# Performance work log

Measured on AMD Instinct MI355X. Metric: run time of the kernel, lower is better.

## Reference

```python
import jax, jax.numpy as jnp
import numpy as np
from jax import lax

HID = 512
NEG = -1e30

def conv2d(x, w, pad):
    # x: [N,C,H,W], w: [O,I,kh,kw]
    return lax.conv_general_dilated(x, w, (1, 1), [(pad, pad), (pad, pad)],
                                    dimension_numbers=('NCHW', 'OIHW', 'NCHW'))

def maxpool3s2p1(x):
    return lax.reduce_window(x, -jnp.inf, lax.max, (1, 1, 3, 3), (1, 1, 2, 2),
                             [(0, 0), (0, 0), (1, 1), (1, 1)])

def setup_inputs() -> dict:
    key = jax.random.key(0)
    ks = jax.random.split(key, 12)
    N, B = 128, 16
    gid = jnp.repeat(jnp.arange(B), N // B).astype(jnp.float32)  # sorted group ids
    rois = jnp.concatenate([gid[:, None], jax.random.uniform(ks[0], (N, 4))], axis=1)
    interact_feat = jax.random.normal(ks[1], (N, 2304, 1, 16, 16), jnp.float32)
    bbox_feat = jax.random.normal(ks[2], (N, 1024, 4, 7, 7), jnp.float32)
    s = lambda k, sh: jax.random.normal(k, sh, jnp.float32) * 0.02
    return {
        'rois': rois,
        'interact_feat': interact_feat,
        'bbox_feat': bbox_feat,
        'w_reduce': s(ks[3], (HID, 2304, 1, 1)),
        'w_rsize': s(ks[4], (HID, HID, 3, 3)),
        'wq': s(ks[5], (HID, HID, 3, 3)),
        'wk': s(ks[6], (HID, HID, 3, 3)),
        'wv': s(ks[7], (HID, HID, 3, 3)),
        'w1': s(ks[8], (HID, HID, 3, 3)),
        'gamma': jnp.ones((HID,), jnp.float32),
        'beta': jnp.zeros((HID,), jnp.float32),
        'w_fc': s(ks[9], (HID, 2 * HID)),
    }

def reference(rois, interact_feat, bbox_feat, w_reduce, w_rsize, wq, wk, wv, w1, gamma, beta, w_fc):
    f = interact_feat[:, :, 0]                      # squeeze(2): [N,2304,16,16]
    f = jax.nn.relu(conv2d(f, w_reduce, 0))         # [N,512,16,16]
    f = conv2d(f, w_rsize, 0)                       # no padding -> [N,512,14,14]
    f = maxpool3s2p1(f)                             # [N,512,7,7]

    gid = rois[:, 0].astype(jnp.int32)
    mask = gid[:, None] == gid[None, :]             # [N,N] same-group mask (vectorizes ragged loop)

    q = conv2d(f, wq, 1)
    k = conv2d(f, wk, 1)
    v = conv2d(f, wv, 1)
    # per-pixel attention across rois within each group
    att = jnp.einsum('ichw,jchw->ijhw', q, k) / jnp.sqrt(jnp.asarray(HID, f.dtype))
    att = jnp.where(mask[:, :, None, None], att, NEG)
    att = jax.nn.softmax(att, axis=1)               # softmax over key rois (dim=1)
    virt = jnp.einsum('ijhw,jchw->ichw', att, v)    # [N,512,7,7]

    # GroupNorm(1, C): normalize over (C,H,W), per-channel affine
    mu = virt.mean(axis=(1, 2, 3), keepdims=True)
    var = virt.var(axis=(1, 2, 3), keepdims=True)
    virt = (virt - mu) / jnp.sqrt(var + 1e-5)
    virt = virt * gamma[None, :, None, None] + beta[None, :, None, None]
    virt = jax.nn.relu(virt)
    virt = conv2d(virt, w1, 1)                      # dropout = identity in eval

    ho = (f + virt).mean(axis=(2, 3))               # gap1 -> [N,512]
    ob = bbox_feat.mean(axis=(2, 3, 4))             # gap2 -> [N,1024]
    ob = jax.nn.relu(ob @ w_fc.T)                   # fc1 -> [N,512]
    return jnp.concatenate([ho, ob], axis=1)        # [N,1024]
```

## Files before the change

kernel.cpp:

```cpp
#include <hip/hip_runtime.h>
#include <hip/hip_bf16.h>
#include <math.h>

typedef __bf16 bf16;
typedef __bf16 v8bf __attribute__((ext_vector_type(8)));
typedef float f32x4 __attribute__((ext_vector_type(4)));

#define GLDS16(g, l) __builtin_amdgcn_global_load_lds( \
    (const __attribute__((address_space(1))) void*)(g), \
    (__attribute__((address_space(3))) void*)(l), 16, 0, 0)

__device__ __forceinline__ int xcd_swz(int bid, int nwg) {
  int xcd = bid & 7, off = bid >> 3;
  int q = nwg >> 3, r = nwg & 7;
  return (xcd < r ? xcd * (q + 1) : r * (q + 1) + (xcd - r) * q) + off;
}

#define SBZ __builtin_amdgcn_sched_barrier(0)
#define BARR __builtin_amdgcn_s_barrier()

#define RD_B8(SLOTB) do { \
  _Pragma("unroll") for (int _j = 0; _j < 4; ++_j) \
  _Pragma("unroll") for (int _kk = 0; _kk < 2; ++_kk) { \
    int _r = (wn & 1) * 64 + _j * 16 + l15; \
    int _c = (_kk * 64 + kq) ^ ((_r & 7) << 4); \
    bfr[_j][_kk] = *(const v8bf*)((SLOTB) + _r * 128 + _c); } } while (0)

#define RD_A4(SLOTA, CL) do { \
  _Pragma("unroll") for (int _f = 0; _f < 2; ++_f) \
  _Pragma("unroll") for (int _kk = 0; _kk < 2; ++_kk) { \
    int _r = (CL) * 32 + _f * 16 + l15; \
    int _c = (_kk * 64 + kq) ^ ((_r & 7) << 4); \
    af[_f][_kk] = *(const v8bf*)((SLOTA) + _r * 128 + _c); } } while (0)

#define MMA16(CL) do { \
  __builtin_amdgcn_s_setprio(1); \
  _Pragma("unroll") for (int _f = 0; _f < 2; ++_f) \
  _Pragma("unroll") for (int _j = 0; _j < 4; ++_j) \
  _Pragma("unroll") for (int _kk = 0; _kk < 2; ++_kk) \
    acc[(CL)*2 + _f][_j] = __builtin_amdgcn_mfma_f32_16x16x32_bf16( \
        af[_f][_kk], bfr[_j][_kk], acc[(CL)*2 + _f][_j], 0, 0, 0); \
  __builtin_amdgcn_s_setprio(0); } while (0)

#define VM4 asm volatile("s_waitcnt vmcnt(4)" ::: "memory")
#define VM0 asm volatile("s_waitcnt vmcnt(0)" ::: "memory")

#define PH8_ITER(STGA, STGB, NIT)                                        \
  {                                                                      \
    int t1k = 2 * iv + 1, t2k = 2 * iv + 2, t3k = 2 * iv + 3;            \
    bool s2 = (iv + 1 < (NIT));                                          \
    RD_B8(bslot0); RD_A4(aslot0, 0); STGA(0, t1k, 1);                    \
    SBZ; BARR; SBZ; MMA16(0); SBZ; BARR;                                 \
    RD_A4(aslot0, 1); STGA(1, t1k, 1);                                   \
    SBZ; BARR; SBZ; MMA16(1); SBZ; BARR;                                 \
    RD_A4(aslot0, 2); if (s2) STGB(0, t2k, 0);                           \
    SBZ; BARR; SBZ; MMA16(2); SBZ; BARR;                                 \
    RD_A4(aslot0, 3); if (s2) STGB(1, t2k, 0);                           \
    SBZ; BARR; SBZ; MMA16(3); SBZ;                                       \
    if (s2) { VM4; } else { VM0; }                                       \
    BARR;                                                                \
    RD_B8(bslot1); RD_A4(aslot1, 0); if (s2) STGA(0, t2k, 0);            \
    SBZ; BARR; SBZ; MMA16(0); SBZ; BARR;                                 \
    RD_A4(aslot1, 1); if (s2) STGA(1, t2k, 0);                           \
    SBZ; BARR; SBZ; MMA16(1); SBZ; BARR;                                 \
    RD_A4(aslot1, 2); if (s2) STGB(0, t3k, 1);                           \
    SBZ; BARR; SBZ; MMA16(2); SBZ; BARR;                                 \
    RD_A4(aslot1, 3); if (s2) STGB(1, t3k, 1);                           \
    SBZ; BARR; SBZ; MMA16(3); SBZ;                                       \
    if (s2) { VM4; } else { VM0; }                                       \
    BARR;                                                                \
  }

__global__ __launch_bounds__(512, 2)
void k_gemm_reduce(const bf16* __restrict__ A, const bf16* __restrict__ B,
                   bf16* __restrict__ f1, int mbase)
{
  extern __shared__ char lds[];
  const int s = xcd_swz(blockIdx.x, gridDim.x);
  const int by = s & 1, bx = s >> 1;
  const int t = threadIdx.x, lane = t & 63, w = t >> 6;
  const int wm = w >> 2, wn = w & 3;
  const int l15 = lane & 15, kq = (lane >> 4) << 4;
  const int tr64 = t >> 3;
  const int lb = ((t & 7) << 4) ^ ((tr64 & 7) << 4);
  const int t16 = t * 16;
  const char* aslot0 = lds + wm * 16384;
  const char* aslot1 = lds + 65536 + wm * 16384;
  const char* bslot0 = lds + 32768 + (wn >> 1) * 16384;
  const char* bslot1 = lds + 98304 + (wn >> 1) * 16384;
  const char* paA[2][2]; const char* paB[2][2];
  #pragma unroll
  for (int h = 0; h < 2; ++h)
    #pragma unroll
    for (int c = 0; c < 2; ++c) {
      paA[h][c] = (const char*)A + (size_t)(bx * 256 + h * 128 + c * 64 + tr64) * 4608 + lb;
      paB[h][c] = (const char*)B + (size_t)(by * 256 + h * 128 + c * 64 + tr64) * 4608 + lb;
    }
  #define GR_STGA(h, kt, d) do { \
    GLDS16(paA[h][0] + (size_t)(kt) * 128, lds + (d) * 65536 + (h) * 16384 + t16); \
    GLDS16(paA[h][1] + (size_t)(kt) * 128, lds + (d) * 65536 + (h) * 16384 + 8192 + t16); } while (0)
  #define GR_STGB(h, kt, d) do { \
    GLDS16(paB[h][0] + (size_t)(kt) * 128, lds + (d) * 65536 + 32768 + (h) * 16384 + t16); \
    GLDS16(paB[h][1] + (size_t)(kt) * 128, lds + (d) * 65536 + 32768 + (h) * 16384 + 8192 + t16); } while (0)

  f32x4 acc[8][4] = {};
  v8bf bfr[4][2], af[2][2];
  GR_STGB(0, 0, 0); GR_STGB(1, 0, 0); GR_STGA(0, 0, 0); GR_STGA(1, 0, 0);
  GR_STGB(0, 1, 1); GR_STGB(1, 1, 1);
  VM4; BARR;
  for (int iv = 0; iv < 18; ++iv) PH8_ITER(GR_STGA, GR_STGB, 18);
  const int rbase = (lane >> 4) << 2, cl = lane & 15;
  #pragma unroll
  for (int i = 0; i < 8; ++i)
    #pragma unroll
    for (int j = 0; j < 4; ++j)
      #pragma unroll
      for (int r = 0; r < 4; ++r) {
        int row = mbase + bx * 256 + wm * 128 + i * 16 + rbase + r;
        int col = by * 256 + wn * 64 + j * 16 + cl;
        f1[(size_t)row * 512 + col] = (bf16)fmaxf(acc[i][j][r], 0.f);
      }
}

__global__ __launch_bounds__(512, 2)
void k_conv_rsize(const bf16* __restrict__ f1, const bf16* __restrict__ wt,
                  bf16* __restrict__ f14)
{
  extern __shared__ char lds[];
  const int s = xcd_swz(blockIdx.x, gridDim.x);
  const int by = s & 1, bx = s >> 1;
  const int t = threadIdx.x, lane = t & 63, w = t >> 6;
  const int wm = w >> 2, wn = w & 3;
  const int l15 = lane & 15, kq = (lane >> 4) << 4;
  const int tr64 = t >> 3;
  const int lb = ((t & 7) << 4) ^ ((tr64 & 7) << 4);
  const int t16 = t * 16;
  const char* aslot0 = lds + wm * 16384;
  const char* aslot1 = lds + 65536 + wm * 16384;
  const char* bslot0 = lds + 32768 + (wn >> 1) * 16384;
  const char* bslot1 = lds + 98304 + (wn >> 1) * 16384;
  int ab[2][2]; const char* pwB[2][2];
  #pragma unroll
  for (int h = 0; h < 2; ++h)
    #pragma unroll
    for (int c = 0; c < 2; ++c) {
      int m = bx * 256 + h * 128 + c * 64 + tr64;
      int n = m / 196, rem = m - n * 196;
      int y = rem / 14, x = rem - 14 * (rem / 14);
      ab[h][c] = n * 256 + y * 16 + x;
      pwB[h][c] = (const char*)wt + (size_t)(by * 256 + h * 128 + c * 64 + tr64) * 1024 + lb;
    }
  const char* f1c = (const char*)f1 + lb;
  #define CR_STGA(h, kt, d) do { \
    int _tap = (kt) >> 3, _ko = ((kt) & 7) << 7; \
    int _dy = (_tap * 11) >> 5, _dx = _tap - _dy * 3; \
    int _df = (_dy * 16 + _dx) << 10; \
    GLDS16(f1c + ((size_t)ab[h][0] << 10) + _df + _ko, lds + (d) * 65536 + (h) * 16384 + t16); \
    GLDS16(f1c + ((size_t)ab[h][1] << 10) + _df + _ko, lds + (d) * 65536 + (h) * 16384 + 8192 + t16); } while (0)
  #define CR_STGB(h, kt, d) do { \
    int _tap = (kt) >> 3, _ko = ((kt) & 7) << 7; \
    GLDS16(pwB[h][0] + (size_t)_tap * 524288 + _ko, lds + (d) * 65536 + 32768 + (h) * 16384 + t16); \
    GLDS16(pwB[h][1] + (size_t)_tap * 524288 + _ko, lds + (d) * 65536 + 32768 + (h) * 16384 + 8192 + t16); } while (0)

  f32x4 acc[8][4] = {};
  v8bf bfr[4][2], af[2][2];
  CR_STGB(0, 0, 0); CR_STGB(1, 0, 0); CR_STGA(0, 0, 0); CR_STGA(1, 0, 0);
  CR_STGB(0, 1, 1); CR_STGB(1, 1, 1);
  VM4; BARR;
  for (int iv = 0; iv < 36; ++iv) PH8_ITER(CR_STGA, CR_STGB, 36);
  const int rbase = (lane >> 4) << 2, cl = lane & 15;
  #pragma unroll
  for (int i = 0; i < 8; ++i)
    #pragma unroll
    for (int j = 0; j < 4; ++j)
      #pragma unroll
      for (int r = 0; r < 4; ++r) {
        int row = bx * 256 + wm * 128 + i * 16 + rbase + r;
        int col = by * 256 + wn * 64 + j * 16 + cl;
        f14[(size_t)row * 512 + col] = (bf16)acc[i][j][r];
      }
}

#define RING_COMPUTE() do { \
  v8bf b_[4], a_[4]; \
  _Pragma("unroll") for (int _j = 0; _j < 4; ++_j) { \
    int _lr = _j * 16 + l15; \
    int _c = (wn * 64 + colb) ^ ((_lr & 7) << 4); \
    b_[_j] = *(const v8bf*)(s0 + 16384 + _lr * 128 + _c); } \
  _Pragma("unroll") for (int _i = 0; _i < 4; ++_i) { \
    int _lr = _i * 16 + l15; \
    int _c = (wm * 64 + colb) ^ ((_lr & 7) << 4); \
    a_[_i] = *(const v8bf*)(s0 + _lr * 128 + _c); } \
  __builtin_amdgcn_s_setprio(1); \
  _Pragma("unroll") for (int _i = 0; _i < 4; ++_i) \
  _Pragma("unroll") for (int _j = 0; _j < 4; ++_j) \
    acc[_i][_j] = __builtin_amdgcn_mfma_f32_16x16x32_bf16(a_[_i], b_[_j], acc[_i][_j], 0, 0, 0); \
  __builtin_amdgcn_s_setprio(0); \
  _Pragma("unroll") for (int _i = 0; _i < 4; ++_i) { \
    int _lr = (_i + 4) * 16 + l15; \
    int _c = (wm * 64 + colb) ^ ((_lr & 7) << 4); \
    a_[_i] = *(const v8bf*)(s0 + _lr * 128 + _c); } \
  __builtin_amdgcn_s_setprio(1); \
  _Pragma("unroll") for (int _i = 0; _i < 4; ++_i) \
  _Pragma("unroll") for (int _j = 0; _j < 4; ++_j) \
    acc[_i + 4][_j] = __builtin_amdgcn_mfma_f32_16x16x32_bf16(a_[_i], b_[_j], acc[_i + 4][_j], 0, 0, 0); \
  __builtin_amdgcn_s_setprio(0); \
} while (0)

#define RING_LOOP(NG, STAGE) do { \
  STAGE(0, s0); STAGE(1, s1); \
  for (int g = 0; g < (NG); ++g) { \
    if (g + 2 < (NG)) { STAGE(g + 2, s2); } \
    if (g + 2 < (NG))       asm volatile("s_waitcnt vmcnt(12)" ::: "memory"); \
    else if (g + 2 == (NG)) asm volatile("s_waitcnt vmcnt(6)" ::: "memory"); \
    else                    asm volatile("s_waitcnt vmcnt(0)" ::: "memory"); \
    __builtin_amdgcn_s_barrier(); \
    __builtin_amdgcn_sched_barrier(0); \
    RING_COMPUTE(); \
    __builtin_amdgcn_sched_barrier(0); \
    __builtin_amdgcn_s_barrier(); \
    char* _tmp = s0; s0 = s1; s1 = s2; s2 = _tmp; \
  } \
} while (0)

__global__ __launch_bounds__(256, 2)
void k_conv_qkv(const bf16* __restrict__ fin, const bf16* __restrict__ wt,
                bf16* __restrict__ qkv, const bf16* __restrict__ zp,
                const float* __restrict__ bbox, float* __restrict__ obm)
{
  __shared__ __attribute__((aligned(16))) char ldss[73728];
  char *s0 = ldss, *s1 = ldss + 24576, *s2 = ldss + 49152;
  const int t = threadIdx.x;
  if (blockIdx.x >= 300) {
    int bid = blockIdx.x - 300;
    int n = bid >> 4;
    int c = (bid & 15) * 64 + (t >> 2);
    int seg = t & 3;
    const float4* p4 = (const float4*)(bbox + ((size_t)n * 1024 + c) * 196);
    float sum = 0.f;
    for (int k = seg; k < 49; k += 4) { float4 ww = p4[k]; sum += ww.x + ww.y + ww.z + ww.w; }
    sum += __shfl_xor(sum, 1);
    sum += __shfl_xor(sum, 2);
    if (seg == 0) obm[n * 1024 + c] = sum * (1.f / 196.f);
    return;
  }
  const int s = xcd_swz(blockIdx.x, 300);
  const int q12 = s % 12, bx = s / 12;
  const int tensor = q12 >> 2, byl = q12 & 3;
  const char* wtc = (const char*)wt + (size_t)tensor * 4718592;
  bf16* outp = qkv + (size_t)tensor * 3211264;
  const int lane = t & 63, w = t >> 6;
  const int wm = w >> 1, wn = w & 1;
  const int l15 = lane & 15, colb = (lane >> 4) << 4;
  const int tr = t >> 3;
  const int lb = ((t & 7) << 4) ^ ((tr & 7) << 4);
  const int hi = lb >> 6, kb = lb & 63;
  const int t16 = t * 16;
  int nb[4], py[4], px[4]; const char* pb[2];
  #pragma unroll
  for (int i = 0; i < 4; ++i) {
    int m = bx * 256 + i * 32 + tr + hi * 128;
    if (m > 6271) m = 6271;
    int n = m / 49, rem = m - n * 49;
    nb[i] = n * 49;
    py[i] = rem / 7 - 1;
    px[i] = rem - 7 * (rem / 7) - 1;
  }
  #pragma unroll
  for (int i = 0; i < 2; ++i)
    pb[i] = wtc + (size_t)(byl * 128 + i * 32 + tr + hi * 64) * 1024 + kb;
  const char* finc = (const char*)fin + kb;
  const char* zpc = (const char*)zp;
  #define SQ(kt, ring) do { int _tap = (kt) >> 4, _ko = ((kt) & 15) << 6; \
    int _dy = (_tap * 11) >> 5, _dx = _tap - _dy * 3; \
    _Pragma("unroll") for (int _i = 0; _i < 4; ++_i) { \
      int _iy = py[_i] + _dy, _ix = px[_i] + _dx; \
      const char* _sp = ((unsigned)_iy < 7u && (unsigned)_ix < 7u) \
          ? finc + (size_t)(nb[_i] + _iy * 7 + _ix) * 1024 + _ko : zpc; \
      GLDS16(_sp, (ring) + _i * 4096 + t16); } \
    _Pragma("unroll") for (int _i = 0; _i < 2; ++_i) \
      GLDS16(pb[_i] + (size_t)_tap * 524288 + _ko, (ring) + 16384 + _i * 4096 + t16); } while (0)
  f32x4 acc[8][4] = {};
  RING_LOOP(144, SQ);
  const int rbase = (lane >> 4) << 2, cl = lane & 15;
  #pragma unroll
  for (int i = 0; i < 8; ++i)
    #pragma unroll
    for (int j = 0; j < 4; ++j)
      #pragma unroll
      for (int r = 0; r < 4; ++r) {
        int row = bx * 256 + wm * 128 + i * 16 + rbase + r;
        if (row < 6272) {
          int col = byl * 128 + wn * 64 + j * 16 + cl;
          outp[(size_t)row * 512 + col] = (bf16)acc[i][j][r];
        }
      }
}

__device__ __forceinline__ void tile_compute(const char* ldsA, const char* ldsB,
                                             f32x4 (&acc)[4][4], int wr, int wc, int lane) {
  const int l15 = lane & 15;
  const int colb = (lane >> 4) << 4;
  #pragma unroll
  for (int kk = 0; kk < 2; ++kk) {
    v8bf a[4], b[4];
    #pragma unroll
    for (int i = 0; i < 4; ++i) {
      int ra = wr * 64 + i * 16 + l15;
      int ca = ((kk << 6) | colb) ^ ((ra & 7) << 4);
      a[i] = *(const v8bf*)(ldsA + ra * 128 + ca);
    }
    #pragma unroll
    for (int j = 0; j < 4; ++j) {
      int rb = wc * 64 + j * 16 + l15;
      int cb = ((kk << 6) | colb) ^ ((rb & 7) << 4);
      b[j] = *(const v8bf*)(ldsB + rb * 128 + cb);
    }
    __builtin_amdgcn_s_setprio(1);
    #pragma unroll
    for (int i = 0; i < 4; ++i)
      #pragma unroll
      for (int j = 0; j < 4; ++j)
        acc[i][j] = __builtin_amdgcn_mfma_f32_16x16x32_bf16(a[i], b[j], acc[i][j], 0, 0, 0);
    __builtin_amdgcn_s_setprio(0);
  }
}

#define PIPELINE_LOOP(NK)                                                   \
  stage(0, lds);                                                            \
  stage(1, lds + 32768);                                                    \
  int cur = 0;                                                              \
  for (int ks = 0; ks < (NK) - 1; ++ks) {                                   \
    asm volatile("s_waitcnt vmcnt(8)" ::: "memory");                        \
    __builtin_amdgcn_s_barrier();                                           \
    __builtin_amdgcn_sched_barrier(0);                                      \
    tile_compute(lds + cur * 32768, lds + cur * 32768 + 16384, acc, wr, wc, lane); \
    __builtin_amdgcn_sched_barrier(0);                                      \
    __builtin_amdgcn_s_barrier();                                           \
    __builtin_amdgcn_sched_barrier(0);                                      \
    if (ks + 2 < (NK)) stage(ks + 2, lds + cur * 32768);                    \
    cur ^= 1;                                                               \
  }                                                                         \
  asm volatile("s_waitcnt vmcnt(0)" ::: "memory");                          \
  __builtin_amdgcn_s_barrier();                                             \
  __builtin_amdgcn_sched_barrier(0);                                        \
  tile_compute(lds + cur * 32768, lds + cur * 32768 + 16384, acc, wr, wc, lane);

__global__ __launch_bounds__(256)
void k_gemm_s(const bf16* __restrict__ A_s, const bf16* __restrict__ w1r,
              float* __restrict__ part)
{
  __shared__ __attribute__((aligned(16))) char lds[65536];
  const int by = blockIdx.x, kspl = blockIdx.y;
  const int t = threadIdx.x, lane = t & 63, w = t >> 6, wr = w >> 1, wc = w & 1;
  const int tr = t >> 3;
  const int cphys = ((t & 7) << 4) ^ ((tr & 7) << 4);
  const char* pa[4]; const char* pb[4];
  #pragma unroll
  for (int i = 0; i < 4; ++i) {
    int r = i * 32 + tr;
    pa[i] = (const char*)A_s + (size_t)r * 9216 + kspl * 2304 + cphys;
    pb[i] = (const char*)w1r + (size_t)(by * 128 + r) * 9216 + kspl * 2304 + cphys;
  }
  const int lo = t * 16;
  auto stage = [&](int ks, char* base) {
    #pragma unroll
    for (int i = 0; i < 4; ++i) GLDS16(pa[i] + ks * 128, base + lo + i * 4096);
    #pragma unroll
    for (int i = 0; i < 4; ++i) GLDS16(pb[i] + ks * 128, base + 16384 + lo + i * 4096);
  };
  f32x4 acc[4][4] = {};
  PIPELINE_LOOP(18)
  const int rb = (lane >> 4) << 2, cl = lane & 15;
  #pragma unroll
  for (int i = 0; i < 4; ++i)
    #pragma unroll
    for (int j = 0; j < 4; ++j)
      #pragma unroll
      for (int r = 0; r < 4; ++r) {
        int row = wr * 64 + i * 16 + rb + r;
        int col = by * 128 + wc * 64 + j * 16 + cl;
        part[(size_t)kspl * 65536 + row * 512 + col] = acc[i][j][r];
      }
}

__global__ __launch_bounds__(512)
void k_red(const float* __restrict__ part, const float* __restrict__ f7m,
           float* __restrict__ out)
{
  int idx = blockIdx.x * 512 + threadIdx.x;
  float s = part[idx] + part[65536 + idx] + part[131072 + idx] + part[196608 + idx];
  int row = idx >> 9, col = idx & 511;
  out[row * 1024 + col] = s + f7m[idx];
}

__global__ void k_tin(const float* __restrict__ in, bf16* __restrict__ A1, int n0)
{
  __shared__ float tile[64][36];
  const int k0 = blockIdx.x * 64, p0 = blockIdx.y * 32, nl = blockIdx.z;
  const int n = n0 + nl;
  const int t = threadIdx.x;
  const float* src = in + (size_t)n * 2304 * 256;
  #pragma unroll
  for (int rep = 0; rep < 2; ++rep) {
    int idx = t + rep * 256;
    int row = idx >> 3, c4 = (idx & 7) * 4;
    float4 v = *(const float4*)(src + (size_t)(k0 + row) * 256 + p0 + c4);
    tile[row][c4] = v.x; tile[row][c4 + 1] = v.y;
    tile[row][c4 + 2] = v.z; tile[row][c4 + 3] = v.w;
  }
  __syncthreads();
  const int pl = t >> 3, ke = (t & 7) * 8;
  v8bf o;
  #pragma unroll
  for (int e = 0; e < 8; ++e) o[e] = (bf16)tile[ke + e][pl];
  bf16* dst = A1 + (size_t)nl * 256 * 2304;
  *(v8bf*)(dst + (size_t)(p0 + pl) * 2304 + k0 + ke) = o;
}

__global__ void k_wprep(const float* __restrict__ wred, const float* __restrict__ s0,
                        const float* __restrict__ s1, const float* __restrict__ s2,
                        const float* __restrict__ s3, const float* __restrict__ s4,
                        bf16* __restrict__ wrb, bf16* __restrict__ wt,
                        bf16* __restrict__ w1r)
{
  if (blockIdx.x < 1152) {
    int idx = (blockIdx.x * 256 + threadIdx.x) * 4;
    float4 v = *(const float4*)(wred + idx);
    bf16* d = wrb + idx;
    d[0] = (bf16)v.x; d[1] = (bf16)v.y; d[2] = (bf16)v.z; d[3] = (bf16)v.w;
    return;
  }
  int bid = blockIdx.x - 1152;
  int by = bid >> 10, bx = bid & 1023;
  const float* src;
  switch (by) {
    case 0: src = s0; break; case 1: src = s1; break; case 2: src = s2; break;
    case 3: src = s3; break; default: src = s4; break;
  }
  int q = bx * 256 + threadIdx.x;
  const float* sp = src + (size_t)q * 9;
  float tmp[9];
  #pragma unroll
  for (int e = 0; e < 9; ++e) tmp[e] = sp[e];
  if (by < 4) {
    bf16* dst = wt + (size_t)by * 2359296;
    #pragma unroll
    for (int e = 0; e < 9; ++e) dst[(size_t)e * 262144 + q] = (bf16)tmp[e];
  } else {
    int co = q >> 9, ci = q & 511;
    #pragma unroll
    for (int e = 0; e < 9; ++e) w1r[(size_t)(co * 9 + e) * 512 + ci] = (bf16)tmp[e];
  }
}

__global__ void k_pool(const bf16* __restrict__ f14, bf16* __restrict__ f7b)
{
  int idx = blockIdx.x * 256 + threadIdx.x;
  int c2 = idx & 255;
  int pp = idx >> 8;
  int n = pp / 49, p7 = pp - n * 49;
  int y = p7 / 7, x = p7 - 7 * (p7 / 7);
  int y0 = 2 * y - 1, x0 = 2 * x - 1;
  const unsigned* f14u = (const unsigned*)f14;
  float m0 = -3.4e38f, m1 = -3.4e38f;
  #pragma unroll
  for (int dy = 0; dy < 3; ++dy) {
    int iy = y0 + dy; if ((unsigned)iy >= 14u) continue;
    #pragma unroll
    for (int dx = 0; dx < 3; ++dx) {
      int ix = x0 + dx; if ((unsigned)ix >= 14u) continue;
      unsigned vv = f14u[(size_t)(n * 196 + iy * 14 + ix) * 256 + c2];
      m0 = fmaxf(m0, __builtin_bit_cast(float, vv << 16));
      m1 = fmaxf(m1, __builtin_bit_cast(float, vv & 0xffff0000u));
    }
  }
  bf16 b0 = (bf16)m0, b1 = (bf16)m1;
  unsigned pk = (unsigned)__builtin_bit_cast(unsigned short, b0)
              | ((unsigned)__builtin_bit_cast(unsigned short, b1) << 16);
  ((unsigned*)f7b)[idx] = pk;
}

__global__ __launch_bounds__(256)
void k_attn(const bf16* __restrict__ q, const bf16* __restrict__ k,
            const bf16* __restrict__ v, const float* __restrict__ rois,
            float* __restrict__ virt)
{
  const int p = blockIdx.x, g = blockIdx.y, t = threadIdx.x;
  __shared__ float sS[8][9];
  __shared__ float sP[8][9];
  __shared__ __attribute__((aligned(16))) bf16 sV[8][512];
  {
    int u = t;
    #pragma unroll
    for (int rep = 0; rep < 2; ++rep, u += 256) {
      int j = u >> 6, ch = u & 63;
      *(v8bf*)&sV[j][ch * 8] = *(const v8bf*)(v + ((size_t)(g * 8 + j) * 49 + p) * 512 + ch * 8);
    }
  }
  int pi = t >> 2, ls = t & 3;
  int i = pi >> 3, j = pi & 7;
  const bf16* qi = q + ((size_t)(g * 8 + i) * 49 + p) * 512;
  const bf16* kj = k + ((size_t)(g * 8 + j) * 49 + p) * 512;
  float s = 0.f;
  for (int ch = ls * 16; ch < ls * 16 + 16; ++ch) {
    v8bf a = *(const v8bf*)(qi + ch * 8);
    v8bf b = *(const v8bf*)(kj + ch * 8);
    #pragma unroll
    for (int e = 0; e < 8; ++e) s += (float)a[e] * (float)b[e];
  }
  s += __shfl_xor(s, 1);
  s += __shfl_xor(s, 2);
  if (ls == 0) sS[i][j] = s * 0.04419417382415922f;
  __syncthreads();
  if (t < 8) {
    float gi = rois[(g * 8 + t) * 5];
    float pv[8]; float mx = -3.4e38f;
    #pragma unroll
    for (int jj = 0; jj < 8; ++jj) {
      float gj = rois[(g * 8 + jj) * 5];
      float sv = (gi == gj) ? sS[t][jj] : -1e30f;
      pv[jj] = sv; mx = fmaxf(mx, sv);
    }
    float sum = 0.f;
    #pragma unroll
    for (int jj = 0; jj < 8; ++jj) { float e = expf(pv[jj] - mx); pv[jj] = e; sum += e; }
    float inv = 1.f / sum;
    #pragma unroll
    for (int jj = 0; jj < 8; ++jj) sP[t][jj] = pv[jj] * inv;
  }
  __syncthreads();
  int i2 = t >> 5, c0 = (t & 31) * 16;
  float o[16];
  #pragma unroll
  for (int e = 0; e < 16; ++e) o[e] = 0.f;
  #pragma unroll
  for (int jj = 0; jj < 8; ++jj) {
    float ww = sP[i2][jj];
    v8bf v0 = *(const v8bf*)&sV[jj][c0];
    v8bf v1 = *(const v8bf*)&sV[jj][c0 + 8];
    #pragma unroll
    for (int e = 0; e < 8; ++e) { o[e] += ww * (float)v0[e]; o[8 + e] += ww * (float)v1[e]; }
  }
  float* dst = virt + ((size_t)(g * 8 + i2) * 49 + p) * 512 + c0;
  #pragma unroll
  for (int e = 0; e < 16; ++e) dst[e] = o[e];
}

__global__ __launch_bounds__(512)
void k_ln_fc(const float* __restrict__ virt, const float* __restrict__ gamma,
             const float* __restrict__ beta, const bf16* __restrict__ f7b,
             bf16* __restrict__ A_s, float* __restrict__ f7m,
             const float* __restrict__ obm, const float* __restrict__ wfc,
             float* __restrict__ out)
{
  const int t = threadIdx.x;
  if (blockIdx.x >= 128) {
    __shared__ float sO[1024];
    int n = blockIdx.x - 128;
    for (int u = t; u < 1024; u += 512) sO[u] = obm[n * 1024 + u];
    __syncthreads();
    const float4* wp = (const float4*)(wfc + (size_t)t * 1024);
    float s = 0.f;
    for (int c4 = 0; c4 < 256; ++c4) {
      float4 w = wp[c4];
      s += w.x * sO[c4 * 4] + w.y * sO[c4 * 4 + 1] + w.z * sO[c4 * 4 + 2] + w.w * sO[c4 * 4 + 3];
    }
    out[n * 1024 + 512 + t] = fmaxf(s, 0.f);
    return;
  }
  const int n = blockIdx.x;
  const float* p = virt + (size_t)n * 25088 + t;
  float xv[49];
  float s1 = 0.f, s2 = 0.f;
  #pragma unroll
  for (int pp = 0; pp < 49; ++pp) {
    float x = p[pp * 512];
    xv[pp] = x; s1 += x; s2 += x * x;
  }
  __shared__ float r1[512], r2[512];
  r1[t] = s1; r2[t] = s2; __syncthreads();
  for (int off = 256; off; off >>= 1) {
    if (t < off) { r1[t] += r1[t + off]; r2[t] += r2[t + off]; }
    __syncthreads();
  }
  float mu = r1[0] * (1.f / 25088.f);
  float var = r2[0] * (1.f / 25088.f) - mu * mu;
  float rstd = rsqrtf(var + 1e-5f);
  float g = gamma[t], be = beta[t];
  const bf16* fp = f7b + (size_t)n * 25088 + t;
  float T = 0, R0 = 0, R6 = 0, C0 = 0, C6 = 0;
  float X00 = 0, X06 = 0, X60 = 0, X66 = 0, F = 0;
  #pragma unroll
  for (int pp = 0; pp < 49; ++pp) {
    const int u = pp / 7, v = pp - 7 * (pp / 7);
    float y = fmaxf((xv[pp] - mu) * rstd * g + be, 0.f);
    T += y;
    if (u == 0) R0 += y;
    if (u == 6) R6 += y;
    if (v == 0) C0 += y;
    if (v == 6) C6 += y;
    if (pp == 0)  X00 = y;
    if (pp == 6)  X06 = y;
    if (pp == 42) X60 = y;
    if (pp == 48) X66 = y;
    F += (float)fp[pp * 512];
  }
  float sv[9] = { T-R6-C6+X66, T-R6, T-R6-C0+X60,
                  T-C6,        T,    T-C0,
                  T-R0-C6+X06, T-R0, T-R0-C0+X00 };
  bf16* Ap = A_s + (size_t)n * 4608 + t;
  #pragma unroll
  for (int tap = 0; tap < 9; ++tap)
    Ap[tap * 512] = (bf16)(sv[tap] * (1.f / 49.f));
  f7m[n * 512 + t] = F * (1.f / 49.f);
}

extern "C" void kernel_launch(void* const* d_in, const int* in_sizes, int n_in,
                              void* d_out, int out_size, void* d_ws, size_t ws_size,
                              hipStream_t stream) {
  const float* rois     = (const float*)d_in[0];
  const float* interact = (const float*)d_in[1];
  const float* bbox     = (const float*)d_in[2];
  const float* w_reduce = (const float*)d_in[3];
  const float* w_rsize  = (const float*)d_in[4];
  const float* wq       = (const float*)d_in[5];
  const float* wk       = (const float*)d_in[6];
  const float* wv       = (const float*)d_in[7];
  const float* w1       = (const float*)d_in[8];
  const float* gamma    = (const float*)d_in[9];
  const float* beta     = (const float*)d_in[10];
  const float* wfc      = (const float*)d_in[11];
  float* out = (float*)d_out;
  char* ws = (char*)d_ws;

  size_t o = 0;
  auto take = [&](size_t sz) { size_t r = o; o += (sz + 255) & ~(size_t)255; return r; };
  bf16*  wrb   = (bf16*)(ws + take(2359296));
  bf16*  wt    = (bf16*)(ws + take(18874368));
  bf16*  w1r   = (bf16*)(ws + take(4718592));
  char*  Rf1   = ws + take(33554432);
  bf16*  f7b   = (bf16*)(ws + take(6422528));
  float* virt  = (float*)(ws + take(12845056));
  bf16*  A_s   = (bf16*)(ws + take(1179648));
  float* f7m   = (float*)(ws + take(262144));
  float* part  = (float*)(ws + take(1048576));
  float* obm   = (float*)(ws + take(524288));
  bf16*  zp    = (bf16*)(ws + take(256));
  size_t fixedEnd = o;
  const size_t A1_FULL = 150994944;
  bool full = (ws_size >= fixedEnd + A1_FULL);
  bf16* A1  = (bf16*)(ws + fixedEnd);
  bf16* f14 = (bf16*)(ws + fixedEnd);

  bf16* f1 = (bf16*)Rf1;
  bf16* qb = (bf16*)Rf1;
  bf16* kb = qb + 3211264;
  bf16* vb = kb + 3211264;

  hipMemsetAsync(zp, 0, 256, stream);

  k_wprep<<<6272, 256, 0, stream>>>(w_reduce, w_rsize, wq, wk, wv, w1, wrb, wt, w1r);

  if (full) {
    k_tin<<<dim3(36, 8, 128), 256, 0, stream>>>(interact, A1, 0);
    k_gemm_reduce<<<256, 512, 131072, stream>>>(A1, wrb, f1, 0);
  } else {
    for (int ch = 0; ch < 4; ++ch) {
      k_tin<<<dim3(36, 8, 32), 256, 0, stream>>>(interact, A1, ch * 32);
      k_gemm_reduce<<<64, 512, 131072, stream>>>(A1, wrb, f1, ch * 8192);
    }
  }

  k_conv_rsize<<<196, 512, 131072, stream>>>(f1, wt, f14);
  k_pool<<<6272, 256, 0, stream>>>(f14, f7b);

  k_conv_qkv<<<2348, 256, 0, stream>>>(f7b, wt + (size_t)1 * 2359296, qb, zp, bbox, obm);

  k_attn<<<dim3(49, 16), 256, 0, stream>>>(qb, kb, vb, rois, virt);

  k_ln_fc<<<256, 512, 0, stream>>>(virt, gamma, beta, f7b, A_s, f7m, obm, wfc, out);

  k_gemm_s<<<dim3(4, 4), 256, 0, stream>>>(A_s, w1r, part);
  k_red<<<128, 512, 0, stream>>>(part, f7m, out);
}
```

Before: 516.3 us.

## Enlarge QKV conv tiles to 256x256 with 8-phase pipeline; fuse split-K reduction via atomics

The QKV 3x3 conv moves from 256x128 tiles with 256 threads and a 3-slot ring to 256x256 tiles with 512 threads and 128KB dynamic LDS, reusing the 8-phase PH8_ITER pipeline already used by the rsize conv. This halves the block count and improves operand reuse per byte loaded. Separately, the split-K partial buffer and the k_red kernel are removed. k_ln_fc now writes the f7 mean directly into the output and k_gemm_s atomically adds its partials on top, which saves a launch and a round trip through memory. The cost is atomic contention and a non-deterministic summation order.

```diff
diff --git a/kernel.cpp b/kernel.cpp
--- a/kernel.cpp
+++ b/kernel.cpp
@@ -181,60 +181,17 @@
       }
 }
 
-#define RING_COMPUTE() do { \
-  v8bf b_[4], a_[4]; \
-  _Pragma("unroll") for (int _j = 0; _j < 4; ++_j) { \
-    int _lr = _j * 16 + l15; \
-    int _c = (wn * 64 + colb) ^ ((_lr & 7) << 4); \
-    b_[_j] = *(const v8bf*)(s0 + 16384 + _lr * 128 + _c); } \
-  _Pragma("unroll") for (int _i = 0; _i < 4; ++_i) { \
-    int _lr = _i * 16 + l15; \
-    int _c = (wm * 64 + colb) ^ ((_lr & 7) << 4); \
-    a_[_i] = *(const v8bf*)(s0 + _lr * 128 + _c); } \
-  __builtin_amdgcn_s_setprio(1); \
-  _Pragma("unroll") for (int _i = 0; _i < 4; ++_i) \
-  _Pragma("unroll") for (int _j = 0; _j < 4; ++_j) \
-    acc[_i][_j] = __builtin_amdgcn_mfma_f32_16x16x32_bf16(a_[_i], b_[_j], acc[_i][_j], 0, 0, 0); \
-  __builtin_amdgcn_s_setprio(0); \
-  _Pragma("unroll") for (int _i = 0; _i < 4; ++_i) { \
-    int _lr = (_i + 4) * 16 + l15; \
-    int _c = (wm * 64 + colb) ^ ((_lr & 7) << 4); \
-    a_[_i] = *(const v8bf*)(s0 + _lr * 128 + _c); } \
-  __builtin_amdgcn_s_setprio(1); \
-  _Pragma("unroll") for (int _i = 0; _i < 4; ++_i) \
-  _Pragma("unroll") for (int _j = 0; _j < 4; ++_j) \
-    acc[_i + 4][_j] = __builtin_amdgcn_mfma_f32_16x16x32_bf16(a_[_i], b_[_j], acc[_i + 4][_j], 0, 0, 0); \
-  __builtin_amdgcn_s_setprio(0); \
-} while (0)
-
-#define RING_LOOP(NG, STAGE) do { \
-  STAGE(0, s0); STAGE(1, s1); \
-  for (int g = 0; g < (NG); ++g) { \
-    if (g + 2 < (NG)) { STAGE(g + 2, s2); } \
-    if (g + 2 < (NG))       asm volatile("s_waitcnt vmcnt(12)" ::: "memory"); \
-    else if (g + 2 == (NG)) asm volatile("s_waitcnt vmcnt(6)" ::: "memory"); \
-    else                    asm volatile("s_waitcnt vmcnt(0)" ::: "memory"); \
-    __builtin_amdgcn_s_barrier(); \
-    __builtin_amdgcn_sched_barrier(0); \
-    RING_COMPUTE(); \
-    __builtin_amdgcn_sched_barrier(0); \
-    __builtin_amdgcn_s_barrier(); \
-    char* _tmp = s0; s0 = s1; s1 = s2; s2 = _tmp; \
-  } \
-} while (0)
-
-__global__ __launch_bounds__(256, 2)
+__global__ __launch_bounds__(512, 2)
 void k_conv_qkv(const bf16* __restrict__ fin, const bf16* __restrict__ wt,
                 bf16* __restrict__ qkv, const bf16* __restrict__ zp,
                 const float* __restrict__ bbox, float* __restrict__ obm)
 {
-  __shared__ __attribute__((aligned(16))) char ldss[73728];
-  char *s0 = ldss, *s1 = ldss + 24576, *s2 = ldss + 49152;
+  extern __shared__ char lds[];
   const int t = threadIdx.x;
-  if (blockIdx.x >= 300) {
-    int bid = blockIdx.x - 300;
-    int n = bid >> 4;
-    int c = (bid & 15) * 64 + (t >> 2);
+  if (blockIdx.x >= 150) {
+    int bid = blockIdx.x - 150;
+    int n = bid >> 3;
+    int c = (bid & 7) * 128 + (t >> 2);
     int seg = t & 3;
     const float4* p4 = (const float4*)(bbox + ((size_t)n * 1024 + c) * 196);
     float sum = 0.f;
@@ -244,44 +201,55 @@
     if (seg == 0) obm[n * 1024 + c] = sum * (1.f / 196.f);
     return;
   }
-  const int s = xcd_swz(blockIdx.x, 300);
-  const int q12 = s % 12, bx = s / 12;
-  const int tensor = q12 >> 2, byl = q12 & 3;
+  const int s = xcd_swz(blockIdx.x, 150);
+  const int q6 = s % 6, bx = s / 6;
+  const int tensor = q6 >> 1, byh = q6 & 1;
   const char* wtc = (const char*)wt + (size_t)tensor * 4718592;
   bf16* outp = qkv + (size_t)tensor * 3211264;
   const int lane = t & 63, w = t >> 6;
-  const int wm = w >> 1, wn = w & 1;
-  const int l15 = lane & 15, colb = (lane >> 4) << 4;
-  const int tr = t >> 3;
-  const int lb = ((t & 7) << 4) ^ ((tr & 7) << 4);
-  const int hi = lb >> 6, kb = lb & 63;
+  const int wm = w >> 2, wn = w & 3;
+  const int l15 = lane & 15, kq = (lane >> 4) << 4;
+  const int tr64 = t >> 3;
+  const int lb = ((t & 7) << 4) ^ ((tr64 & 7) << 4);
   const int t16 = t * 16;
-  int nb[4], py[4], px[4]; const char* pb[2];
-  #pragma unroll
-  for (int i = 0; i < 4; ++i) {
-    int m = bx * 256 + i * 32 + tr + hi * 128;
-    if (m > 6271) m = 6271;
-    int n = m / 49, rem = m - n * 49;
-    nb[i] = n * 49;
-    py[i] = rem / 7 - 1;
-    px[i] = rem - 7 * (rem / 7) - 1;
-  }
-  #pragma unroll
-  for (int i = 0; i < 2; ++i)
-    pb[i] = wtc + (size_t)(byl * 128 + i * 32 + tr + hi * 64) * 1024 + kb;
-  const char* finc = (const char*)fin + kb;
+  const char* aslot0 = lds + wm * 16384;
+  const char* aslot1 = lds + 65536 + wm * 16384;
+  const char* bslot0 = lds + 32768 + (wn >> 1) * 16384;
+  const char* bslot1 = lds + 98304 + (wn >> 1) * 16384;
+  int nb[2][2], py[2][2], px[2][2]; const char* pwB[2][2];
+  #pragma unroll
+  for (int h = 0; h < 2; ++h)
+    #pragma unroll
+    for (int c = 0; c < 2; ++c) {
+      int m = bx * 256 + h * 128 + c * 64 + tr64;
+      if (m > 6271) m = 6271;
+      int n = m / 49, rem = m - n * 49;
+      nb[h][c] = n * 49;
+      py[h][c] = rem / 7 - 1;
+      px[h][c] = rem - 7 * (rem / 7) - 1;
+      pwB[h][c] = wtc + (size_t)(byh * 256 + h * 128 + c * 64 + tr64) * 1024 + lb;
+    }
+  const char* finc = (const char*)fin + lb;
   const char* zpc = (const char*)zp;
-  #define SQ(kt, ring) do { int _tap = (kt) >> 4, _ko = ((kt) & 15) << 6; \
+  #define QK_STGA(h, kt, d) do { \
+    int _tap = (kt) >> 3, _ko = ((kt) & 7) << 7; \
     int _dy = (_tap * 11) >> 5, _dx = _tap - _dy * 3; \
-    _Pragma("unroll") for (int _i = 0; _i < 4; ++_i) { \
-      int _iy = py[_i] + _dy, _ix = px[_i] + _dx; \
+    _Pragma("unroll") for (int _c = 0; _c < 2; ++_c) { \
+      int _iy = py[h][_c] + _dy, _ix = px[h][_c] + _dx; \
       const char* _sp = ((unsigned)_iy < 7u && (unsigned)_ix < 7u) \
-          ? finc + (size_t)(nb[_i] + _iy * 7 + _ix) * 1024 + _ko : zpc; \
-      GLDS16(_sp, (ring) + _i * 4096 + t16); } \
-    _Pragma("unroll") for (int _i = 0; _i < 2; ++_i) \
-      GLDS16(pb[_i] + (size_t)_tap * 524288 + _ko, (ring) + 16384 + _i * 4096 + t16); } while (0)
+          ? finc + (size_t)(nb[h][_c] + _iy * 7 + _ix) * 1024 + _ko : zpc; \
+      GLDS16(_sp, lds + (d) * 65536 + (h) * 16384 + _c * 8192 + t16); } } while (0)
+  #define QK_STGB(h, kt, d) do { \
+    int _tap = (kt) >> 3, _ko = ((kt) & 7) << 7; \
+    GLDS16(pwB[h][0] + (size_t)_tap * 524288 + _ko, lds + (d) * 65536 + 32768 + (h) * 16384 + t16); \
+    GLDS16(pwB[h][1] + (size_t)_tap * 524288 + _ko, lds + (d) * 65536 + 32768 + (h) * 16384 + 8192 + t16); } while (0)
+
   f32x4 acc[8][4] = {};
-  RING_LOOP(144, SQ);
+  v8bf bfr[4][2], af[2][2];
+  QK_STGB(0, 0, 0); QK_STGB(1, 0, 0); QK_STGA(0, 0, 0); QK_STGA(1, 0, 0);
+  QK_STGB(0, 1, 1); QK_STGB(1, 1, 1);
+  VM4; BARR;
+  for (int iv = 0; iv < 36; ++iv) PH8_ITER(QK_STGA, QK_STGB, 36);
   const int rbase = (lane >> 4) << 2, cl = lane & 15;
   #pragma unroll
   for (int i = 0; i < 8; ++i)
@@ -291,7 +259,7 @@
       for (int r = 0; r < 4; ++r) {
         int row = bx * 256 + wm * 128 + i * 16 + rbase + r;
         if (row < 6272) {
-          int col = byl * 128 + wn * 64 + j * 16 + cl;
+          int col = byh * 256 + wn * 64 + j * 16 + cl;
           outp[(size_t)row * 512 + col] = (bf16)acc[i][j][r];
         }
       }
@@ -348,7 +316,7 @@
 
 __global__ __launch_bounds__(256)
 void k_gemm_s(const bf16* __restrict__ A_s, const bf16* __restrict__ w1r,
-              float* __restrict__ part)
+              float* __restrict__ out)
 {
   __shared__ __attribute__((aligned(16))) char lds[65536];
   const int by = blockIdx.x, kspl = blockIdx.y;
@@ -380,18 +348,8 @@
       for (int r = 0; r < 4; ++r) {
         int row = wr * 64 + i * 16 + rb + r;
         int col = by * 128 + wc * 64 + j * 16 + cl;
-        part[(size_t)kspl * 65536 + row * 512 + col] = acc[i][j][r];
+        atomicAdd(&out[(size_t)row * 1024 + col], acc[i][j][r]);
       }
-}
-
-__global__ __launch_bounds__(512)
-void k_red(const float* __restrict__ part, const float* __restrict__ f7m,
-           float* __restrict__ out)
-{
-  int idx = blockIdx.x * 512 + threadIdx.x;
-  float s = part[idx] + part[65536 + idx] + part[131072 + idx] + part[196608 + idx];
-  int row = idx >> 9, col = idx & 511;
-  out[row * 1024 + col] = s + f7m[idx];
 }
 
 __global__ void k_tin(const float* __restrict__ in, bf16* __restrict__ A1, int n0)
@@ -550,7 +508,7 @@
 __global__ __launch_bounds__(512)
 void k_ln_fc(const float* __restrict__ virt, const float* __restrict__ gamma,
              const float* __restrict__ beta, const bf16* __restrict__ f7b,
-             bf16* __restrict__ A_s, float* __restrict__ f7m,
+             bf16* __restrict__ A_s,
              const float* __restrict__ obm, const float* __restrict__ wfc,
              float* __restrict__ out)
 {
@@ -613,7 +571,7 @@
   #pragma unroll
   for (int tap = 0; tap < 9; ++tap)
     Ap[tap * 512] = (bf16)(sv[tap] * (1.f / 49.f));
-  f7m[n * 512 + t] = F * (1.f / 49.f);
+  out[n * 1024 + t] = F * (1.f / 49.f);
 }
 
 extern "C" void kernel_launch(void* const* d_in, const int* in_sizes, int n_in,
@@ -643,8 +601,6 @@
   bf16*  f7b   = (bf16*)(ws + take(6422528));
   float* virt  = (float*)(ws + take(12845056));
   bf16*  A_s   = (bf16*)(ws + take(1179648));
-  float* f7m   = (float*)(ws + take(262144));
-  float* part  = (float*)(ws + take(1048576));
   float* obm   = (float*)(ws + take(524288));
   bf16*  zp    = (bf16*)(ws + take(256));
   size_t fixedEnd = o;
@@ -675,12 +631,11 @@
   k_conv_rsize<<<196, 512, 131072, stream>>>(f1, wt, f14);
   k_pool<<<6272, 256, 0, stream>>>(f14, f7b);
 
-  k_conv_qkv<<<2348, 256, 0, stream>>>(f7b, wt + (size_t)1 * 2359296, qb, zp, bbox, obm);
+  k_conv_qkv<<<1174, 512, 131072, stream>>>(f7b, wt + (size_t)1 * 2359296, qb, zp, bbox, obm);
 
   k_attn<<<dim3(49, 16), 256, 0, stream>>>(qb, kb, vb, rois, virt);
 
-  k_ln_fc<<<256, 512, 0, stream>>>(virt, gamma, beta, f7b, A_s, f7m, obm, wfc, out);
-
-  k_gemm_s<<<dim3(4, 4), 256, 0, stream>>>(A_s, w1r, part);
-  k_red<<<128, 512, 0, stream>>>(part, f7m, out);
-}
+  k_ln_fc<<<256, 512, 0, stream>>>(virt, gamma, beta, f7b, A_s, obm, wfc, out);
+
+  k_gemm_s<<<dim3(4, 4), 256, 0, stream>>>(A_s, w1r, out);
+}
```

After: 514.7 us, median of 2. No clear change (-0.3%).
